# Kernel tuning notes

Hardware: AMD Instinct MI355X
Metric: run time of the kernel (lower is better)

The kernel has to match this reference:

```python
import jax, jax.numpy as jnp
import numpy as np
from jax import lax

B, CIN, H, W = 1, 1024, 48, 160
FEAT = 64            # PSM_features
D = 48               # depth_channel = max_disp / downsample_scale
EPS = 1e-5


def _bn(x, g, b, m, v, ndim):
    # eval-mode batchnorm over channel axis 1
    shape = (1, -1) + (1,) * (ndim - 2)
    return (x - m.reshape(shape)) * (g.reshape(shape) * lax.rsqrt(v.reshape(shape) + EPS)) + b.reshape(shape)


def _conv3d(x, w, b):
    y = lax.conv_general_dilated(x, w, (1, 1, 1), 'SAME',
                                 dimension_numbers=('NCDHW', 'OIDHW', 'NCDHW'))
    return y + b[None, :, None, None, None]


def setup_inputs() -> dict:
    key = jax.random.key(0)
    ks = jax.random.split(key, 24)
    f32 = jnp.float32
    inp = {}
    inp['left_features'] = jax.random.normal(ks[0], (B, CIN, H, W), f32)
    inp['right_features'] = jax.random.normal(ks[1], (B, CIN, H, W), f32)
    # 1x1 down_sample conv + BN2d
    inp['ds_w'] = jax.random.normal(ks[2], (FEAT, CIN), f32) * (1.0 / np.sqrt(CIN))
    inp['ds_b'] = jax.random.normal(ks[3], (FEAT,), f32) * 0.01
    inp['bn2_g'] = jax.random.uniform(ks[4], (FEAT,), f32, 0.9, 1.1)
    inp['bn2_b'] = jax.random.normal(ks[5], (FEAT,), f32) * 0.01
    inp['bn2_m'] = jax.random.normal(ks[6], (FEAT,), f32) * 0.01
    inp['bn2_v'] = jax.random.uniform(ks[7], (FEAT,), f32, 0.5, 1.5)
    # conv3d block 1: 2*FEAT -> FEAT, 3x3x3
    inp['c3a_w'] = jax.random.normal(ks[8], (FEAT, 2 * FEAT, 3, 3, 3), f32) * (1.0 / np.sqrt(2 * FEAT * 27))
    inp['c3a_b'] = jax.random.normal(ks[9], (FEAT,), f32) * 0.01
    inp['bn3a_g'] = jax.random.uniform(ks[10], (FEAT,), f32, 0.9, 1.1)
    inp['bn3a_b'] = jax.random.normal(ks[11], (FEAT,), f32) * 0.01
    inp['bn3a_m'] = jax.random.normal(ks[12], (FEAT,), f32) * 0.01
    inp['bn3a_v'] = jax.random.uniform(ks[13], (FEAT,), f32, 0.5, 1.5)
    # conv3d block 2: FEAT -> FEAT, 3x3x3
    inp['c3b_w'] = jax.random.normal(ks[14], (FEAT, FEAT, 3, 3, 3), f32) * (1.0 / np.sqrt(FEAT * 27))
    inp['c3b_b'] = jax.random.normal(ks[15], (FEAT,), f32) * 0.01
    inp['bn3b_g'] = jax.random.uniform(ks[16], (FEAT,), f32, 0.9, 1.1)
    inp['bn3b_b'] = jax.random.normal(ks[17], (FEAT,), f32) * 0.01
    inp['bn3b_m'] = jax.random.normal(ks[18], (FEAT,), f32) * 0.01
    inp['bn3b_v'] = jax.random.uniform(ks[19], (FEAT,), f32, 0.5, 1.5)
    return inp


def reference(left_features, right_features, ds_w, ds_b, bn2_g, bn2_b, bn2_m, bn2_v,
              c3a_w, c3a_b, bn3a_g, bn3a_b, bn3a_m, bn3a_v,
              c3b_w, c3b_b, bn3b_g, bn3b_b, bn3b_m, bn3b_v):
    def down_sample(x):
        y = jnp.einsum('bchw,oc->bohw', x, ds_w) + ds_b[None, :, None, None]
        return jax.nn.relu(_bn(y, bn2_g, bn2_b, bn2_m, bn2_v, 4))

    left = down_sample(left_features)    # [B,FEAT,H,W]
    right = down_sample(right_features)  # [B,FEAT,H,W]

    # Cost volume: for disparity i, left copied at w>=i, right shifted right by i.
    d_idx = jnp.arange(D)[:, None]        # [D,1]
    w_idx = jnp.arange(W)[None, :]        # [1,W]
    mask = (w_idx >= d_idx).astype(left.dtype)          # [D,W]
    cost_left = left[:, :, None, :, :] * mask[None, None, :, None, :]  # [B,F,D,H,W]
    shift = jnp.clip(w_idx - d_idx, 0, W - 1)           # [D,W], right[..., w-i]
    right_g = right[:, :, :, shift]                     # [B,F,H,D,W]
    cost_right = jnp.transpose(right_g, (0, 1, 3, 2, 4)) * mask[None, None, :, None, :]
    cost = jnp.concatenate([cost_left, cost_right], axis=1)  # [B,2F,D,H,W]

    y = jax.nn.relu(_bn(_conv3d(cost, c3a_w, c3a_b), bn3a_g, bn3a_b, bn3a_m, bn3a_v, 5))
    y = jax.nn.relu(_bn(_conv3d(y, c3b_w, c3b_b), bn3b_g, bn3b_b, bn3b_m, bn3b_v, 5))
    return y.reshape(B, -1, H, W)  # [B, FEAT*D, H, W]
```

## Files before the change

### kernel.cpp

```cpp
#include <hip/hip_runtime.h>
#include <hip/hip_bf16.h>

#define CIN   1024
#define FEATN 64
#define HH    48
#define WW    160
#define DDN   48
#define EPSV  1e-5f
#define NTAP  27
#define WSLAB 162

typedef __attribute__((ext_vector_type(8))) short bf16x8;
typedef __attribute__((ext_vector_type(4))) float f32x4;
typedef __attribute__((ext_vector_type(4))) unsigned short u16x4;

static __device__ __forceinline__ unsigned short f2bf(float x) {
    __hip_bfloat16 h = __float2bfloat16(x);
    return *(unsigned short*)&h;
}

__global__ void CostVolume_6201932775918_packw(const float* w3, unsigned short* Wb)
{
    int i = (int)(blockIdx.x * 256 + threadIdx.x);
    if (i >= 64 * NTAP * 128) return;
    int ci  = i & 127;
    int tap = (i >> 7) % NTAP;
    int o   = i / (NTAP * 128);
    Wb[i] = f2bf(w3[o * 3456 + ci * 27 + tap]);
}

__global__ void CostVolume_6201932775918_packw2(const float* w3, unsigned short* Wb2)
{
    int i = (int)(blockIdx.x * 256 + threadIdx.x);
    if (i >= 64 * NTAP * 64) return;
    int ci  = i & 63;
    int tap = (i >> 6) % NTAP;
    int o   = i / (NTAP * 64);
    Wb2[i] = f2bf(w3[o * 1728 + ci * 27 + tap]);
}

__global__ void CostVolume_6201932775918_ds(
    const float* Lf, const float* Rf,
    const float* dsw, const float* dsb,
    const float* g2, const float* b2, const float* m2, const float* v2,
    unsigned short* outL, unsigned short* outR)
{
    const float* in = (blockIdx.y == 0) ? Lf : Rf;
    unsigned short* out = (blockIdx.y == 0) ? outL : outR;
    const int t    = (int)threadIdx.x;
    const int pos0 = (int)blockIdx.x * 64;
    const int oq   = t & 15;
    const int pq   = t >> 4;

    __shared__ float chunk[64 * 64];

    float acc[4][4];
    #pragma unroll
    for (int k = 0; k < 4; ++k)
        #pragma unroll
        for (int j = 0; j < 4; ++j) acc[k][j] = 0.f;

    for (int cc = 0; cc < 16; ++cc) {
        __syncthreads();
        #pragma unroll
        for (int i = 0; i < 16; ++i) {
            int idx = i * 256 + t;
            int cl = idx >> 6;
            int p  = idx & 63;
            chunk[cl * 64 + p] = in[(cc * 64 + cl) * (HH * WW) + pos0 + p];
        }
        __syncthreads();
        for (int cl = 0; cl < 64; ++cl) {
            int c = cc * 64 + cl;
            float x0 = chunk[cl * 64 + pq * 4 + 0];
            float x1 = chunk[cl * 64 + pq * 4 + 1];
            float x2 = chunk[cl * 64 + pq * 4 + 2];
            float x3 = chunk[cl * 64 + pq * 4 + 3];
            #pragma unroll
            for (int k = 0; k < 4; ++k) {
                float w = dsw[(4 * oq + k) * CIN + c];
                acc[k][0] = fmaf(w, x0, acc[k][0]);
                acc[k][1] = fmaf(w, x1, acc[k][1]);
                acc[k][2] = fmaf(w, x2, acc[k][2]);
                acc[k][3] = fmaf(w, x3, acc[k][3]);
            }
        }
    }

    float s4[4], cb4[4];
    #pragma unroll
    for (int k = 0; k < 4; ++k) {
        int o = 4 * oq + k;
        s4[k]  = g2[o] / sqrtf(v2[o] + EPSV);
        cb4[k] = dsb[o] * s4[k] + b2[o] - m2[o] * s4[k];
    }
    #pragma unroll
    for (int j = 0; j < 4; ++j) {
        u16x4 v;
        #pragma unroll
        for (int k = 0; k < 4; ++k)
            v[k] = f2bf(fmaxf(0.f, fmaf(acc[k][j], s4[k], cb4[k])));
        *(u16x4*)&out[(size_t)(pos0 + pq * 4 + j) * 64 + 4 * oq] = v;
    }
}

__global__ __launch_bounds__(256) void CostVolume_6201932775918_c3a(
    const unsigned short* Lt, const unsigned short* Rt,
    const unsigned short* Wb,
    const float* cb3, const float* g3, const float* b3,
    const float* m3, const float* v3,
    unsigned short* y1t)
{
    const int h    = (int)blockIdx.x;
    const int d    = (int)blockIdx.y;
    const int t    = (int)threadIdx.x;
    const int wave = t >> 6;
    const int lane = t & 63;
    const int l15  = lane & 15;
    const int lhi  = lane >> 4;

    __shared__ __align__(16) unsigned short slab[WSLAB * 128];

    f32x4 acc[10];
    #pragma unroll
    for (int n = 0; n < 10; ++n) acc[n] = (f32x4){0.f, 0.f, 0.f, 0.f};

    char* slabB = (char*)slab;

    for (int kd = 0; kd < 3; ++kd) {
        const int dp = d + kd - 1;
        if (dp < 0 || dp >= DDN) continue;
        for (int kh = 0; kh < 3; ++kh) {
            const int hp = h + kh - 1;
            if (hp < 0 || hp >= HH) continue;
            __syncthreads();
            const unsigned short* Lrow = Lt + (size_t)hp * WW * 64;
            const unsigned short* Rrow = Rt + ((size_t)hp * WW - (size_t)dp) * 64;
            #pragma unroll
            for (int i = 0; i < 11; ++i) {
                int e = i * 256 + t;
                if (e < WSLAB * 16) {
                    int wIdx = e >> 4;
                    int c16  = e & 15;
                    int wp   = wIdx - 1;
                    u16x4 v0 = (u16x4){0, 0, 0, 0}, v1 = (u16x4){0, 0, 0, 0};
                    if (wp >= dp && wp < WW) {
                        const unsigned short* src =
                            (c16 < 8) ? (Lrow + (size_t)wp * 64 + c16 * 8)
                                      : (Rrow + (size_t)wp * 64 + (c16 - 8) * 8);
                        v0 = *(const u16x4*)src;
                        v1 = *(const u16x4*)(src + 4);
                    }
                    int byte = (wIdx * 256 + c16 * 16) ^ ((wIdx & 15) << 4);
                    *(u16x4*)(slabB + byte)     = v0;
                    *(u16x4*)(slabB + byte + 8) = v1;
                }
            }
            __syncthreads();
            const int tapbase = (kd * 3 + kh) * 3;
            #pragma unroll
            for (int kw = 0; kw < 3; ++kw) {
                const unsigned short* wrow =
                    Wb + (16 * wave + l15) * (NTAP * 128) + (tapbase + kw) * 128 + lhi * 8;
                #pragma unroll
                for (int kc = 0; kc < 4; ++kc) {
                    bf16x8 afrag = *(const bf16x8*)(wrow + kc * 32);
                    const int ci0x2 = (kc * 32 + lhi * 8) * 2;
                    #pragma unroll
                    for (int n = 0; n < 10; ++n) {
                        int wIdx = 16 * n + l15 + kw;
                        int byte = (wIdx * 256 + ci0x2) ^ ((wIdx & 15) << 4);
                        bf16x8 bfrag = *(const bf16x8*)(slabB + byte);
                        acc[n] = __builtin_amdgcn_mfma_f32_16x16x32_bf16(
                            afrag, bfrag, acc[n], 0, 0, 0);
                    }
                }
            }
        }
    }

    float s4[4], cb4[4];
    #pragma unroll
    for (int r = 0; r < 4; ++r) {
        const int o = 16 * wave + lhi * 4 + r;
        s4[r]  = g3[o] / sqrtf(v3[o] + EPSV);
        cb4[r] = cb3[o] * s4[r] + b3[o] - m3[o] * s4[r];
    }
    unsigned short* ybase =
        y1t + ((size_t)(d * HH + h) * WW) * 64 + 16 * wave + lhi * 4;
    #pragma unroll
    for (int n = 0; n < 10; ++n) {
        int w = 16 * n + l15;
        u16x4 v;
        #pragma unroll
        for (int r = 0; r < 4; ++r)
            v[r] = f2bf(fmaxf(0.f, fmaf(acc[n][r], s4[r], cb4[r])));
        *(u16x4*)(ybase + (size_t)w * 64) = v;
    }
}

__global__ __launch_bounds__(256) void CostVolume_6201932775918_c3b(
    const unsigned short* y1t, const unsigned short* Wb2,
    const float* cb3, const float* g3, const float* b3,
    const float* m3, const float* v3,
    float* outp)
{
    const int h    = (int)blockIdx.x;
    const int d    = (int)blockIdx.y;
    const int t    = (int)threadIdx.x;
    const int wave = t >> 6;
    const int lane = t & 63;
    const int l15  = lane & 15;
    const int lhi  = lane >> 4;

    __shared__ __align__(16) unsigned short S[2][WSLAB * 64];

    f32x4 acc[10];
    #pragma unroll
    for (int n = 0; n < 10; ++n) acc[n] = (f32x4){0.f, 0.f, 0.f, 0.f};

    int buf = 0;

    for (int kd = 0; kd < 3; ++kd) {
        const int dp = d + kd - 1;
        if (dp < 0 || dp >= DDN) continue;
        for (int kh = 0; kh < 3; ++kh) {
            const int hp = h + kh - 1;
            if (hp < 0 || hp >= HH) continue;
            char* SB = (char*)S[buf];
            const unsigned short* yrow = y1t + ((size_t)(dp * HH + hp) * WW) * 64;
            #pragma unroll
            for (int i = 0; i < 6; ++i) {
                int e = i * 256 + t;
                if (e < WSLAB * 8) {
                    int wIdx = e >> 3, c8 = e & 7, wp = wIdx - 1;
                    u16x4 v0 = (u16x4){0, 0, 0, 0}, v1 = (u16x4){0, 0, 0, 0};
                    if (wp >= 0 && wp < WW) {
                        const unsigned short* src = yrow + (size_t)wp * 64 + c8 * 8;
                        v0 = *(const u16x4*)src;
                        v1 = *(const u16x4*)(src + 4);
                    }
                    int byte = (wIdx * 128 + c8 * 16) ^ ((wIdx & 7) << 4);
                    *(u16x4*)(SB + byte)     = v0;
                    *(u16x4*)(SB + byte + 8) = v1;
                }
            }
            __syncthreads();
            const int tap0 = (kd * 3 + kh) * 3;
            #pragma unroll
            for (int kw = 0; kw < 3; ++kw) {
                const unsigned short* wrow =
                    Wb2 + (16 * wave + l15) * (NTAP * 64) + (tap0 + kw) * 64 + lhi * 8;
                #pragma unroll
                for (int kc = 0; kc < 2; ++kc) {
                    bf16x8 afrag = *(const bf16x8*)(wrow + kc * 32);
                    const int ci2 = (kc * 32 + lhi * 8) * 2;
                    #pragma unroll
                    for (int n = 0; n < 10; ++n) {
                        int wIdx = 16 * n + l15 + kw;
                        int byte = (wIdx * 128 + ci2) ^ ((wIdx & 7) << 4);
                        bf16x8 b = *(const bf16x8*)(SB + byte);
                        acc[n] = __builtin_amdgcn_mfma_f32_16x16x32_bf16(
                            afrag, b, acc[n], 0, 0, 0);
                    }
                }
            }
            buf ^= 1;
        }
    }

    float s4[4], cb4[4];
    #pragma unroll
    for (int r = 0; r < 4; ++r) {
        const int o = 16 * wave + lhi * 4 + r;
        s4[r]  = g3[o] / sqrtf(v3[o] + EPSV);
        cb4[r] = cb3[o] * s4[r] + b3[o] - m3[o] * s4[r];
    }
    #pragma unroll
    for (int r = 0; r < 4; ++r) {
        const int o = 16 * wave + lhi * 4 + r;
        float* orow = outp + ((size_t)(o * DDN + d) * HH + h) * WW;
        #pragma unroll
        for (int n = 0; n < 10; ++n) {
            int w = 16 * n + l15;
            orow[w] = fmaxf(0.f, fmaf(acc[n][r], s4[r], cb4[r]));
        }
    }
}

extern "C" void kernel_launch(void* const* d_in, const int* in_sizes, int n_in,
                              void* d_out, int out_size, void* d_ws, size_t ws_size,
                              hipStream_t stream)
{
    (void)in_sizes; (void)n_in; (void)out_size;

    const float* Lf  = (const float*)d_in[0];
    const float* Rf  = (const float*)d_in[1];
    const float* dsw = (const float*)d_in[2];
    const float* dsb = (const float*)d_in[3];
    const float* g2  = (const float*)d_in[4];
    const float* b2  = (const float*)d_in[5];
    const float* m2  = (const float*)d_in[6];
    const float* v2  = (const float*)d_in[7];
    const float* w3a = (const float*)d_in[8];
    const float* cba = (const float*)d_in[9];
    const float* g3a = (const float*)d_in[10];
    const float* b3a = (const float*)d_in[11];
    const float* m3a = (const float*)d_in[12];
    const float* v3a = (const float*)d_in[13];
    const float* w3b = (const float*)d_in[14];
    const float* cbb = (const float*)d_in[15];
    const float* g3b = (const float*)d_in[16];
    const float* b3b = (const float*)d_in[17];
    const float* m3b = (const float*)d_in[18];
    const float* v3b = (const float*)d_in[19];

    float* outF = (float*)d_out;

    unsigned short* Lt  = (unsigned short*)d_ws;
    unsigned short* Rt  = (unsigned short*)((char*)d_ws + 983040);
    unsigned short* Wb  = (unsigned short*)((char*)d_ws + 1966080);
    unsigned short* Wb2 = (unsigned short*)((char*)d_ws + 2408448);
    unsigned short* y1t = (unsigned short*)((char*)d_ws + 2629632);
    if (ws_size < 2629632 + (size_t)DDN * HH * WW * 64 * 2) return;

    CostVolume_6201932775918_packw<<<dim3(864), 256, 0, stream>>>(w3a, Wb);
    CostVolume_6201932775918_packw2<<<dim3(432), 256, 0, stream>>>(w3b, Wb2);

    CostVolume_6201932775918_ds<<<dim3(120, 2), 256, 0, stream>>>(
        Lf, Rf, dsw, dsb, g2, b2, m2, v2, Lt, Rt);

    CostVolume_6201932775918_c3a<<<dim3(48, 48), 256, 0, stream>>>(
        Lt, Rt, Wb, cba, g3a, b3a, m3a, v3a, y1t);

    CostVolume_6201932775918_c3b<<<dim3(48, 48), 256, 0, stream>>>(
        y1t, Wb2, cbb, g3b, b3b, m3b, v3b, outF);
}
```

Baseline: 477.6 us.

## Stage conv slabs with direct global-to-LDS loads and double-buffer c3b

Both 3D conv kernels now fill their shared-memory slabs with global_load_lds 16-byte transfers that skip registers. Each lane picks a pre-swizzled source address, and padding lanes read from a small zeroed buffer. In c3b, a precomputed list of valid taps lets the kernel prefetch the next (kd,kh) slab into the other buffer while MFMAs run on the current one, which should hide load latency. The cost is reliance on async LDS-load semantics: correctness depends on the swizzled lane-to-address mapping and on the sync placement.

After: 435.2 us, median of 2. 1.1x faster.

```diff
diff --git a/kernel.cpp b/kernel.cpp
--- a/kernel.cpp
+++ b/kernel.cpp
@@ -19,6 +19,14 @@
     return *(unsigned short*)&h;
 }
 
+static __device__ __forceinline__ void gld16(const void* g, void* l)
+{
+    __builtin_amdgcn_global_load_lds(
+        (const __attribute__((address_space(1))) void*)g,
+        (__attribute__((address_space(3))) void*)l,
+        16, 0, 0);
+}
+
 __global__ void CostVolume_6201932775918_packw(const float* w3, unsigned short* Wb)
 {
     int i = (int)(blockIdx.x * 256 + threadIdx.x);
@@ -29,8 +37,10 @@
     Wb[i] = f2bf(w3[o * 3456 + ci * 27 + tap]);
 }
 
-__global__ void CostVolume_6201932775918_packw2(const float* w3, unsigned short* Wb2)
-{
+__global__ void CostVolume_6201932775918_packw2(const float* w3, unsigned short* Wb2,
+                                                unsigned short* Zb)
+{
+    if (blockIdx.x == 0 && threadIdx.x < 32) Zb[threadIdx.x] = 0;
     int i = (int)(blockIdx.x * 256 + threadIdx.x);
     if (i >= 64 * NTAP * 64) return;
     int ci  = i & 63;
@@ -106,7 +116,7 @@
 
 __global__ __launch_bounds__(256) void CostVolume_6201932775918_c3a(
     const unsigned short* Lt, const unsigned short* Rt,
-    const unsigned short* Wb,
+    const unsigned short* Wb, const unsigned short* Zb,
     const float* cb3, const float* g3, const float* b3,
     const float* m3, const float* v3,
     unsigned short* y1t)
@@ -138,22 +148,17 @@
             const unsigned short* Rrow = Rt + ((size_t)hp * WW - (size_t)dp) * 64;
             #pragma unroll
             for (int i = 0; i < 11; ++i) {
-                int e = i * 256 + t;
+                int witer = i * 4 + wave;
+                int e = witer * 64 + lane;
                 if (e < WSLAB * 16) {
                     int wIdx = e >> 4;
-                    int c16  = e & 15;
+                    int c16  = (e & 15) ^ (wIdx & 15);
                     int wp   = wIdx - 1;
-                    u16x4 v0 = (u16x4){0, 0, 0, 0}, v1 = (u16x4){0, 0, 0, 0};
-                    if (wp >= dp && wp < WW) {
-                        const unsigned short* src =
-                            (c16 < 8) ? (Lrow + (size_t)wp * 64 + c16 * 8)
-                                      : (Rrow + (size_t)wp * 64 + (c16 - 8) * 8);
-                        v0 = *(const u16x4*)src;
-                        v1 = *(const u16x4*)(src + 4);
-                    }
-                    int byte = (wIdx * 256 + c16 * 16) ^ ((wIdx & 15) << 4);
-                    *(u16x4*)(slabB + byte)     = v0;
-                    *(u16x4*)(slabB + byte + 8) = v1;
+                    const unsigned short* src = Zb;
+                    if (wp >= dp && wp < WW)
+                        src = (c16 < 8) ? (Lrow + (size_t)wp * 64 + c16 * 8)
+                                        : (Rrow + (size_t)wp * 64 + (c16 - 8) * 8);
+                    gld16(src, slabB + (size_t)witer * 1024);
                 }
             }
             __syncthreads();
@@ -201,6 +206,7 @@
 
 __global__ __launch_bounds__(256) void CostVolume_6201932775918_c3b(
     const unsigned short* y1t, const unsigned short* Wb2,
+    const unsigned short* Zb,
     const float* cb3, const float* g3, const float* b3,
     const float* m3, const float* v3,
     float* outp)
@@ -219,54 +225,63 @@
     #pragma unroll
     for (int n = 0; n < 10; ++n) acc[n] = (f32x4){0.f, 0.f, 0.f, 0.f};
 
+    const int kd0 = (d == 0) ? 1 : 0;
+    const int kd1 = (d == DDN - 1) ? 1 : 2;
+    const int kh0 = (h == 0) ? 1 : 0;
+    const int kh1 = (h == HH - 1) ? 1 : 2;
+    const int nh  = kh1 - kh0 + 1;
+    const int P   = (kd1 - kd0 + 1) * nh;
+
+    auto stage_b = [&](int p, int buf) {
+        int kd = kd0 + p / nh;
+        int kh = kh0 + p % nh;
+        int dp = d + kd - 1, hp = h + kh - 1;
+        const unsigned short* yrow = y1t + ((size_t)(dp * HH + hp) * WW) * 64;
+        char* SB = (char*)S[buf];
+        #pragma unroll
+        for (int i = 0; i < 6; ++i) {
+            int witer = i * 4 + wave;
+            int e = witer * 64 + lane;
+            if (e < WSLAB * 8) {
+                int wIdx = e >> 3;
+                int c8   = (e & 7) ^ (wIdx & 7);
+                int wp   = wIdx - 1;
+                const unsigned short* src = Zb;
+                if (wp >= 0 && wp < WW)
+                    src = yrow + (size_t)wp * 64 + c8 * 8;
+                gld16(src, SB + (size_t)witer * 1024);
+            }
+        }
+    };
+
+    stage_b(0, 0);
     int buf = 0;
-
-    for (int kd = 0; kd < 3; ++kd) {
-        const int dp = d + kd - 1;
-        if (dp < 0 || dp >= DDN) continue;
-        for (int kh = 0; kh < 3; ++kh) {
-            const int hp = h + kh - 1;
-            if (hp < 0 || hp >= HH) continue;
-            char* SB = (char*)S[buf];
-            const unsigned short* yrow = y1t + ((size_t)(dp * HH + hp) * WW) * 64;
+    for (int p = 0; p < P; ++p) {
+        __syncthreads();
+        if (p + 1 < P) stage_b(p + 1, buf ^ 1);
+        int kd = kd0 + p / nh;
+        int kh = kh0 + p % nh;
+        const int tap0 = (kd * 3 + kh) * 3;
+        char* SB = (char*)S[buf];
+        #pragma unroll
+        for (int kw = 0; kw < 3; ++kw) {
+            const unsigned short* wrow =
+                Wb2 + (16 * wave + l15) * (NTAP * 64) + (tap0 + kw) * 64 + lhi * 8;
             #pragma unroll
-            for (int i = 0; i < 6; ++i) {
-                int e = i * 256 + t;
-                if (e < WSLAB * 8) {
-                    int wIdx = e >> 3, c8 = e & 7, wp = wIdx - 1;
-                    u16x4 v0 = (u16x4){0, 0, 0, 0}, v1 = (u16x4){0, 0, 0, 0};
-                    if (wp >= 0 && wp < WW) {
-                        const unsigned short* src = yrow + (size_t)wp * 64 + c8 * 8;
-                        v0 = *(const u16x4*)src;
-                        v1 = *(const u16x4*)(src + 4);
-                    }
-                    int byte = (wIdx * 128 + c8 * 16) ^ ((wIdx & 7) << 4);
-                    *(u16x4*)(SB + byte)     = v0;
-                    *(u16x4*)(SB + byte + 8) = v1;
+            for (int kc = 0; kc < 2; ++kc) {
+                bf16x8 afrag = *(const bf16x8*)(wrow + kc * 32);
+                const int ci2 = (kc * 32 + lhi * 8) * 2;
+                #pragma unroll
+                for (int n = 0; n < 10; ++n) {
+                    int wIdx = 16 * n + l15 + kw;
+                    int byte = (wIdx * 128 + ci2) ^ ((wIdx & 7) << 4);
+                    bf16x8 b = *(const bf16x8*)(SB + byte);
+                    acc[n] = __builtin_amdgcn_mfma_f32_16x16x32_bf16(
+                        afrag, b, acc[n], 0, 0, 0);
                 }
             }
-            __syncthreads();
-            const int tap0 = (kd * 3 + kh) * 3;
-            #pragma unroll
-            for (int kw = 0; kw < 3; ++kw) {
-                const unsigned short* wrow =
-                    Wb2 + (16 * wave + l15) * (NTAP * 64) + (tap0 + kw) * 64 + lhi * 8;
-                #pragma unroll
-                for (int kc = 0; kc < 2; ++kc) {
-                    bf16x8 afrag = *(const bf16x8*)(wrow + kc * 32);
-                    const int ci2 = (kc * 32 + lhi * 8) * 2;
-                    #pragma unroll
-                    for (int n = 0; n < 10; ++n) {
-                        int wIdx = 16 * n + l15 + kw;
-                        int byte = (wIdx * 128 + ci2) ^ ((wIdx & 7) << 4);
-                        bf16x8 b = *(const bf16x8*)(SB + byte);
-                        acc[n] = __builtin_amdgcn_mfma_f32_16x16x32_bf16(
-                            afrag, b, acc[n], 0, 0, 0);
-                    }
-                }
-            }
-            buf ^= 1;
-        }
+        }
+        buf ^= 1;
     }
 
     float s4[4], cb4[4];
@@ -322,17 +337,18 @@
     unsigned short* Wb  = (unsigned short*)((char*)d_ws + 1966080);
     unsigned short* Wb2 = (unsigned short*)((char*)d_ws + 2408448);
     unsigned short* y1t = (unsigned short*)((char*)d_ws + 2629632);
-    if (ws_size < 2629632 + (size_t)DDN * HH * WW * 64 * 2) return;
+    unsigned short* Zb  = (unsigned short*)((char*)d_ws + 49815552);
+    if (ws_size < 49815552 + 64) return;
 
     CostVolume_6201932775918_packw<<<dim3(864), 256, 0, stream>>>(w3a, Wb);
-    CostVolume_6201932775918_packw2<<<dim3(432), 256, 0, stream>>>(w3b, Wb2);
+    CostVolume_6201932775918_packw2<<<dim3(432), 256, 0, stream>>>(w3b, Wb2, Zb);
 
     CostVolume_6201932775918_ds<<<dim3(120, 2), 256, 0, stream>>>(
         Lf, Rf, dsw, dsb, g2, b2, m2, v2, Lt, Rt);
 
     CostVolume_6201932775918_c3a<<<dim3(48, 48), 256, 0, stream>>>(
-        Lt, Rt, Wb, cba, g3a, b3a, m3a, v3a, y1t);
+        Lt, Rt, Wb, Zb, cba, g3a, b3a, m3a, v3a, y1t);
 
     CostVolume_6201932775918_c3b<<<dim3(48, 48), 256, 0, stream>>>(
-        y1t, Wb2, cbb, g3b, b3b, m3b, v3b, outF);
-}
+        y1t, Wb2, Zb, cbb, g3b, b3b, m3b, v3b, outF);
+}
```
